# Performance work log

Measured on AMD Instinct MI355X. Metric: run time of the kernel, lower is better.

Reference implementation:

```python
import jax, jax.numpy as jnp
import numpy as np
import math

D = 768
H = 12
DK = D // H
DI = 3072
EPS_LN = 1e-12
NEG = -1e9


def layernorm(x, g, b):
    mu = jnp.mean(x, axis=-1, keepdims=True)
    var = jnp.mean(jnp.square(x - mu), axis=-1, keepdims=True)
    return (x - mu) * jax.lax.rsqrt(var + EPS_LN) * g + b


def setup_inputs() -> dict:
    key = jax.random.key(0)
    ks = jax.random.split(key, 16)
    B, S = 16, 512
    sd = 0.02
    inp = {
        "hidden_states": jax.random.normal(ks[0], (B, S, D), dtype=jnp.float32),
        "constituent_prior": jnp.zeros((B, S, S), dtype=jnp.float32),
        "attention_mask": jnp.ones((B, S), dtype=jnp.int32),
        # MultiHeadedAttention: 4 linears (q, k, v, out)
        "Wq": jax.random.normal(ks[1], (D, D)) * sd, "bq": jnp.zeros((D,)),
        "Wk": jax.random.normal(ks[2], (D, D)) * sd, "bk": jnp.zeros((D,)),
        "Wv": jax.random.normal(ks[3], (D, D)) * sd, "bv": jnp.zeros((D,)),
        "Wo": jax.random.normal(ks[4], (D, D)) * sd, "bo": jnp.zeros((D,)),
        # GroupAttention: key/query linears + LayerNorm
        "gWk": jax.random.normal(ks[5], (D, D)) * sd, "gbk": jnp.zeros((D,)),
        "gWq": jax.random.normal(ks[6], (D, D)) * sd, "gbq": jnp.zeros((D,)),
        "g_ln_g": jnp.ones((D,)), "g_ln_b": jnp.zeros((D,)),
        # BertIntermediate / BertOutput
        "Wi": jax.random.normal(ks[7], (D, DI)) * sd, "bi": jnp.zeros((DI,)),
        "Wout": jax.random.normal(ks[8], (DI, D)) * sd, "bout": jnp.zeros((D,)),
        "ln_g": jnp.ones((D,)), "ln_b": jnp.zeros((D,)),
    }
    return {k: v.astype(jnp.float32) if v.dtype == jnp.float32 or jnp.issubdtype(v.dtype, jnp.floating) else v for k, v in inp.items()}


def group_attention(x, attention_mask, prior, gWk, gbk, gWq, gbq, g_ln_g, g_ln_b):
    B, S, _ = x.shape
    a = jnp.eye(S, k=1, dtype=jnp.float32)      # super-diagonal
    c = jnp.eye(S, k=-1, dtype=jnp.float32)     # sub-diagonal
    eye = jnp.eye(S, dtype=jnp.float32)
    tri = jnp.triu(jnp.ones((S, S), dtype=jnp.float32))  # upper-tri incl. diag

    h = layernorm(x, g_ln_g, g_ln_b)
    k = h @ gWk + gbk
    q = h @ gWq + gbq
    scores = jnp.einsum("bsd,btd->bst", q, k) / D
    # mask[b,i,j] = attention_mask[b,j] & (a+c)[i,j]  (only +/-1 neighbors)
    mask = attention_mask.astype(jnp.float32)[:, None, :] * (a + c)[None]
    scores = jnp.where(mask == 0, NEG, scores)
    neigh = jax.nn.softmax(scores, axis=-1)
    neigh = jnp.sqrt(neigh * jnp.swapaxes(neigh, -2, -1) + 1e-9)
    neigh = prior + (1.0 - prior) * neigh

    # prefix log-sums along the super-diagonal via triangular matmuls
    t = jnp.where(a[None] == 0, 0.0, jnp.log(neigh + 1e-9)) @ tri
    C = jnp.exp(jnp.einsum("ij,bjk->bik", tri, t))
    C = jnp.where((tri - eye)[None] == 0, 0.0, C)   # keep strictly upper tri
    C = C + jnp.swapaxes(C, -2, -1) + jnp.where(eye[None] == 0, 1e-9, neigh)
    return C, neigh


def multi_head_attention(x, group_prob, attention_mask, Wq, bq, Wk, bk, Wv, bv, Wo, bo):
    B, S, _ = x.shape
    def split(y):  # [B,S,D] -> [B,H,S,DK]
        return y.reshape(B, S, H, DK).transpose(0, 2, 1, 3)
    q = split(x @ Wq + bq)
    k = split(x @ Wk + bk)
    v = split(x @ Wv + bv)
    scores = jnp.einsum("bhsd,bhtd->bhst", q, k) / math.sqrt(DK)
    eye = jnp.eye(S, dtype=jnp.int32)
    # combined mask: allow key j if attention_mask[b,j] or j == i (diagonal)
    cm = (attention_mask[:, None, None, :] | eye[None, None]) != 0
    scores = jnp.where(cm, scores, NEG)
    p = jax.nn.softmax(scores, axis=-1) * group_prob[:, None]  # [B,H,S,S]
    out = jnp.einsum("bhst,bhtd->bhsd", p, v)
    out = out.transpose(0, 2, 1, 3).reshape(B, S, D)
    return out @ Wo + bo


def reference(hidden_states, constituent_prior, attention_mask,
              Wq, bq, Wk, bk, Wv, bv, Wo, bo,
              gWk, gbk, gWq, gbq, g_ln_g, g_ln_b,
              Wi, bi, Wout, bout, ln_g, ln_b):
    C, neigh = group_attention(hidden_states, attention_mask, constituent_prior,
                               gWk, gbk, gWq, gbq, g_ln_g, g_ln_b)
    attn_out = multi_head_attention(hidden_states, C, attention_mask,
                                    Wq, bq, Wk, bk, Wv, bv, Wo, bo)
    inter = jax.nn.gelu(attn_out @ Wi + bi, approximate=False)
    layer_out = layernorm(inter @ Wout + bout + attn_out, ln_g, ln_b)
    return (layer_out, C, neigh, attn_out)
```

## Files before the change

### kernel.cpp

```cpp
#include <hip/hip_runtime.h>
#include <math.h>

typedef unsigned short ushort_t;
typedef __attribute__((ext_vector_type(8))) short bf16x8;
typedef __attribute__((ext_vector_type(4))) float f32x4;

#define Dt 768
#define Mrows 8192

__device__ __forceinline__ ushort_t f2b(float f) {
    union { float f; unsigned int u; } v; v.f = f;
    unsigned int u = v.u;
    unsigned int r = (u + 0x7fffu + ((u >> 16) & 1u)) >> 16;
    return (ushort_t)r;
}
__device__ __forceinline__ float b2f(ushort_t u) {
    union { unsigned int u; float f; } v; v.u = ((unsigned int)u) << 16;
    return v.f;
}
__device__ __forceinline__ f32x4 mfma16(bf16x8 a, bf16x8 b, f32x4 c) {
    return __builtin_amdgcn_mfma_f32_16x16x32_bf16(a, b, c, 0, 0, 0);
}
__device__ __forceinline__ float gelu_exact(float v) {
    return 0.5f * v * (1.0f + erff(v * 0.70710678118654752f));
}
__device__ __forceinline__ void gl2lds16(const ushort_t* g, ushort_t* l) {
    __builtin_amdgcn_global_load_lds((const __attribute__((address_space(1))) void*)g,
                                     (__attribute__((address_space(3))) void*)l,
                                     16, 0, 0);
}

__global__ __launch_bounds__(256)
void tconv6_kernel(const float* i0, const float* i1, const float* i2,
                   const float* i3, const float* i4, const float* i5,
                   ushort_t* o0, ushort_t* o1, ushort_t* o2,
                   ushort_t* o3, ushort_t* o4, ushort_t* o5)
{
    const float* in; ushort_t* out;
    switch (blockIdx.z) {
        case 0: in = i0; out = o0; break;
        case 1: in = i1; out = o1; break;
        case 2: in = i2; out = o2; break;
        case 3: in = i3; out = o3; break;
        case 4: in = i4; out = o4; break;
        default: in = i5; out = o5; break;
    }
    __shared__ float T[32][33];
    int t = threadIdx.x;
    int n0 = blockIdx.x * 32, k0 = blockIdx.y * 32;
    int r = t >> 3, c4 = (t & 7) * 4;
    float4 v = *(const float4*)(in + (size_t)(k0 + r) * 768 + n0 + c4);
    T[r][c4] = v.x; T[r][c4 + 1] = v.y; T[r][c4 + 2] = v.z; T[r][c4 + 3] = v.w;
    __syncthreads();
    int nl = t >> 3, k4 = (t & 7) * 4;
    unsigned int lo = (unsigned int)f2b(T[k4][nl]) | ((unsigned int)f2b(T[k4 + 1][nl]) << 16);
    unsigned int hi = (unsigned int)f2b(T[k4 + 2][nl]) | ((unsigned int)f2b(T[k4 + 3][nl]) << 16);
    uint2 o; o.x = lo; o.y = hi;
    *(uint2*)(out + (size_t)(n0 + nl) * 768 + k0 + k4) = o;
}

__global__ __launch_bounds__(256)
void tconv_kernel(const float* __restrict__ in, ushort_t* __restrict__ out,
                  int K, int N)
{
    __shared__ float T[32][33];
    int t = threadIdx.x;
    int n0 = blockIdx.x * 32, k0 = blockIdx.y * 32;
    int r = t >> 3, c4 = (t & 7) * 4;
    float4 v = *(const float4*)(in + (size_t)(k0 + r) * N + n0 + c4);
    T[r][c4] = v.x; T[r][c4 + 1] = v.y; T[r][c4 + 2] = v.z; T[r][c4 + 3] = v.w;
    __syncthreads();
    int nl = t >> 3, k4 = (t & 7) * 4;
    unsigned int lo = (unsigned int)f2b(T[k4][nl]) | ((unsigned int)f2b(T[k4 + 1][nl]) << 16);
    unsigned int hi = (unsigned int)f2b(T[k4 + 2][nl]) | ((unsigned int)f2b(T[k4 + 3][nl]) << 16);
    uint2 o; o.x = lo; o.y = hi;
    *(uint2*)(out + (size_t)(n0 + nl) * K + k0 + k4) = o;
}

__global__ __launch_bounds__(256)
void bconcat_kernel(const float* bq, const float* bk, const float* bv,
                    const float* gbq, const float* gbk,
                    float* bqkv, float* gbqk)
{
    int g = blockIdx.x * 256 + threadIdx.x;
    if (g < 768)       bqkv[g] = bq[g];
    else if (g < 1536) bqkv[g] = bk[g - 768];
    else if (g < 2304) bqkv[g] = bv[g - 1536];
    else if (g < 3072) gbqk[g - 2304] = gbq[g - 2304];
    else if (g < 3840) gbqk[g - 2304] = gbk[g - 3072];
}

__global__ __launch_bounds__(256)
void lnx_kernel(const float* __restrict__ x, const float* __restrict__ g,
                const float* __restrict__ be, ushort_t* __restrict__ xb,
                ushort_t* __restrict__ hb)
{
    int row = blockIdx.x;
    const float* xr = x + (size_t)row * Dt;
    int t = threadIdx.x;
    float v0 = xr[t], v1 = xr[t + 256], v2 = xr[t + 512];
    ushort_t* xrow = xb + (size_t)row * Dt;
    xrow[t] = f2b(v0); xrow[t + 256] = f2b(v1); xrow[t + 512] = f2b(v2);
    float s = v0 + v1 + v2;
    #pragma unroll
    for (int off = 32; off; off >>= 1) s += __shfl_xor(s, off, 64);
    __shared__ float r1[4], r2[4];
    if ((t & 63) == 0) r1[t >> 6] = s;
    __syncthreads();
    float mu = (r1[0] + r1[1] + r1[2] + r1[3]) * (1.0f / Dt);
    float d0 = v0 - mu, d1 = v1 - mu, d2 = v2 - mu;
    float sq = d0 * d0 + d1 * d1 + d2 * d2;
    #pragma unroll
    for (int off = 32; off; off >>= 1) sq += __shfl_xor(sq, off, 64);
    if ((t & 63) == 0) r2[t >> 6] = sq;
    __syncthreads();
    float var = (r2[0] + r2[1] + r2[2] + r2[3]) * (1.0f / Dt);
    float rs = 1.0f / sqrtf(var + 1e-12f);
    ushort_t* hrow = hb + (size_t)row * Dt;
    hrow[t]       = f2b(d0 * rs * g[t]       + be[t]);
    hrow[t + 256] = f2b(d1 * rs * g[t + 256] + be[t + 256]);
    hrow[t + 512] = f2b(d2 * rs * g[t + 512] + be[t + 512]);
}

__global__ __launch_bounds__(256)
void ln_kernel(const float* __restrict__ x, const float* __restrict__ g,
               const float* __restrict__ be, float* __restrict__ out)
{
    int row = blockIdx.x;
    const float* xr = x + (size_t)row * Dt;
    int t = threadIdx.x;
    float v0 = xr[t], v1 = xr[t + 256], v2 = xr[t + 512];
    float s = v0 + v1 + v2;
    #pragma unroll
    for (int off = 32; off; off >>= 1) s += __shfl_xor(s, off, 64);
    __shared__ float r1[4], r2[4];
    if ((t & 63) == 0) r1[t >> 6] = s;
    __syncthreads();
    float mu = (r1[0] + r1[1] + r1[2] + r1[3]) * (1.0f / Dt);
    float d0 = v0 - mu, d1 = v1 - mu, d2 = v2 - mu;
    float sq = d0 * d0 + d1 * d1 + d2 * d2;
    #pragma unroll
    for (int off = 32; off; off >>= 1) sq += __shfl_xor(sq, off, 64);
    if ((t & 63) == 0) r2[t >> 6] = sq;
    __syncthreads();
    float var = (r2[0] + r2[1] + r2[2] + r2[3]) * (1.0f / Dt);
    float rs = 1.0f / sqrtf(var + 1e-12f);
    float* orow = out + (size_t)row * Dt;
    orow[t]       = d0 * rs * g[t]       + be[t];
    orow[t + 256] = d1 * rs * g[t + 256] + be[t + 256];
    orow[t + 512] = d2 * rs * g[t + 512] + be[t + 512];
}

enum { EPI_BF16 = 1, EPI_QKV = 2, EPI_DUAL = 3, EPI_GELU = 4, EPI_RES = 5, EPI_ACC = 6 };

template<int BN, int EPI>
__global__ __launch_bounds__(256)
void gemm128(const ushort_t* __restrict__ A, const ushort_t* __restrict__ Bt,
             const float* __restrict__ bias, const float* __restrict__ res,
             float* __restrict__ Cf, ushort_t* __restrict__ O0,
             ushort_t* __restrict__ O1, ushort_t* __restrict__ O2,
             int K, int ldb, int ldc)
{
    constexpr int NF = BN / 32;
    __shared__ ushort_t As[128 * 32];
    __shared__ ushort_t Bs[BN * 32];
    int t = threadIdx.x;
    int w = t >> 6, l = t & 63;
    int wr = w >> 1, wc = w & 1;
    int lr = l & 15, lg = l >> 4;
    int bn = blockIdx.x * BN;
    int bm = blockIdx.y * 128;

    const ushort_t* gA0 = A + (size_t)(bm + (t >> 2)) * K + ((t & 3) << 3);
    const ushort_t* gA1 = A + (size_t)(bm + 64 + (t >> 2)) * K + ((t & 3) << 3);
    const ushort_t* gB0 = Bt + (size_t)(bn + (t >> 2)) * ldb + ((t & 3) << 3);
    const ushort_t* gB1 = (BN == 128) ?
        Bt + (size_t)(bn + 64 + (t >> 2)) * ldb + ((t & 3) << 3) : nullptr;
    ushort_t* lA0 = As + (w << 9);
    ushort_t* lA1 = As + 2048 + (w << 9);
    ushort_t* lB0 = Bs + (w << 9);
    ushort_t* lB1 = Bs + 2048 + (w << 9);

    f32x4 acc[4][NF];
    #pragma unroll
    for (int m = 0; m < 4; ++m)
        #pragma unroll
        for (int n = 0; n < NF; ++n) acc[m][n] = (f32x4)0.0f;

    for (int k0 = 0; k0 < K; k0 += 32) {
        gl2lds16(gA0 + k0, lA0);
        gl2lds16(gA1 + k0, lA1);
        gl2lds16(gB0 + k0, lB0);
        if (BN == 128) gl2lds16(gB1 + k0, lB1);
        __syncthreads();
        bf16x8 af[4], bfv[NF];
        #pragma unroll
        for (int m = 0; m < 4; ++m)
            af[m] = *(const bf16x8*)&As[(wr * 64 + m * 16 + lr) * 32 + lg * 8];
        #pragma unroll
        for (int n = 0; n < NF; ++n)
            bfv[n] = *(const bf16x8*)&Bs[(wc * (BN / 2) + n * 16 + lr) * 32 + lg * 8];
        __builtin_amdgcn_s_setprio(1);
        #pragma unroll
        for (int m = 0; m < 4; ++m)
            #pragma unroll
            for (int n = 0; n < NF; ++n)
                acc[m][n] = mfma16(af[m], bfv[n], acc[m][n]);
        __builtin_amdgcn_s_setprio(0);
        __syncthreads();
    }

    #pragma unroll
    for (int m = 0; m < 4; ++m) {
        int row0 = bm + wr * 64 + m * 16 + lg * 4;
        #pragma unroll
        for (int n = 0; n < NF; ++n) {
            int ng = bn + wc * (BN / 2) + n * 16 + lr;
            float v0 = acc[m][n][0], v1 = acc[m][n][1];
            float v2 = acc[m][n][2], v3 = acc[m][n][3];
            if (EPI != EPI_ACC) {
                float bv = bias[ng];
                v0 += bv; v1 += bv; v2 += bv; v3 += bv;
            }
            if (EPI == EPI_BF16) {
                O0[(size_t)(row0 + 0) * ldc + ng] = f2b(v0);
                O0[(size_t)(row0 + 1) * ldc + ng] = f2b(v1);
                O0[(size_t)(row0 + 2) * ldc + ng] = f2b(v2);
                O0[(size_t)(row0 + 3) * ldc + ng] = f2b(v3);
            } else if (EPI == EPI_QKV) {
                if (bn < 768) {
                    O0[(size_t)(row0 + 0) * 768 + ng] = f2b(v0 * 0.125f);
                    O0[(size_t)(row0 + 1) * 768 + ng] = f2b(v1 * 0.125f);
                    O0[(size_t)(row0 + 2) * 768 + ng] = f2b(v2 * 0.125f);
                    O0[(size_t)(row0 + 3) * 768 + ng] = f2b(v3 * 0.125f);
                } else if (bn < 1536) {
                    int c = ng - 768;
                    O1[(size_t)(row0 + 0) * 768 + c] = f2b(v0);
                    O1[(size_t)(row0 + 1) * 768 + c] = f2b(v1);
                    O1[(size_t)(row0 + 2) * 768 + c] = f2b(v2);
                    O1[(size_t)(row0 + 3) * 768 + c] = f2b(v3);
                } else {
                    int dk = ng - 1536;
                    unsigned int lo = (unsigned int)f2b(v0) | ((unsigned int)f2b(v1) << 16);
                    unsigned int hi = (unsigned int)f2b(v2) | ((unsigned int)f2b(v3) << 16);
                    uint2 o; o.x = lo; o.y = hi;
                    *(uint2*)(O2 + (size_t)dk * Mrows + row0) = o;
                }
            } else if (EPI == EPI_DUAL) {
                Cf[(size_t)(row0 + 0) * ldc + ng] = v0;
                Cf[(size_t)(row0 + 1) * ldc + ng] = v1;
                Cf[(size_t)(row0 + 2) * ldc + ng] = v2;
                Cf[(size_t)(row0 + 3) * ldc + ng] = v3;
                O0[(size_t)(row0 + 0) * ldc + ng] = f2b(v0);
                O0[(size_t)(row0 + 1) * ldc + ng] = f2b(v1);
                O0[(size_t)(row0 + 2) * ldc + ng] = f2b(v2);
                O0[(size_t)(row0 + 3) * ldc + ng] = f2b(v3);
            } else if (EPI == EPI_GELU) {
                O0[(size_t)(row0 + 0) * ldc + ng] = f2b(gelu_exact(v0));
                O0[(size_t)(row0 + 1) * ldc + ng] = f2b(gelu_exact(v1));
                O0[(size_t)(row0 + 2) * ldc + ng] = f2b(gelu_exact(v2));
                O0[(size_t)(row0 + 3) * ldc + ng] = f2b(gelu_exact(v3));
            } else if (EPI == EPI_RES) {
                Cf[(size_t)(row0 + 0) * ldc + ng] = v0 + res[(size_t)(row0 + 0) * Dt + ng];
                Cf[(size_t)(row0 + 1) * ldc + ng] = v1 + res[(size_t)(row0 + 1) * Dt + ng];
                Cf[(size_t)(row0 + 2) * ldc + ng] = v2 + res[(size_t)(row0 + 2) * Dt + ng];
                Cf[(size_t)(row0 + 3) * ldc + ng] = v3 + res[(size_t)(row0 + 3) * Dt + ng];
            } else if (EPI == EPI_ACC) {
                Cf[(size_t)(row0 + 0) * ldc + ng] += v0;
                Cf[(size_t)(row0 + 1) * ldc + ng] += v1;
                Cf[(size_t)(row0 + 2) * ldc + ng] += v2;
                Cf[(size_t)(row0 + 3) * ldc + ng] += v3;
            }
        }
    }
}

__global__ __launch_bounds__(256)
void group_scores_kernel(const ushort_t* __restrict__ GQK, const int* __restrict__ am,
                         float* __restrict__ smU, float* __restrict__ smD,
                         int* __restrict__ emptyF)
{
    int gi = blockIdx.x;
    int b = gi >> 9, s = gi & 511;
    int t = threadIdx.x;
    const ushort_t* qr = GQK + (size_t)gi * 1536;
    bool hasU = (s < 511) && (am[(b << 9) + s + 1] != 0);
    bool hasD = (s > 0)   && (am[(b << 9) + s - 1] != 0);
    float su = 0.0f, sd = 0.0f;
    if (hasU) {
        const ushort_t* kr = GQK + (size_t)(gi + 1) * 1536 + 768;
        for (int c = t; c < Dt; c += 256) su += b2f(qr[c]) * b2f(kr[c]);
    }
    if (hasD) {
        const ushort_t* kr = GQK + (size_t)(gi - 1) * 1536 + 768;
        for (int c = t; c < Dt; c += 256) sd += b2f(qr[c]) * b2f(kr[c]);
    }
    #pragma unroll
    for (int off = 32; off; off >>= 1) { su += __shfl_xor(su, off, 64); sd += __shfl_xor(sd, off, 64); }
    __shared__ float rU[4], rD[4];
    if ((t & 63) == 0) { rU[t >> 6] = su; rD[t >> 6] = sd; }
    __syncthreads();
    if (t == 0) {
        su = (rU[0] + rU[1] + rU[2] + rU[3]) * (1.0f / Dt);
        sd = (rD[0] + rD[1] + rD[2] + rD[3]) * (1.0f / Dt);
        float u, d2; int emp = 0;
        if (hasU && hasD) {
            float m = fmaxf(su, sd);
            float eu = __expf(su - m), ed = __expf(sd - m);
            float inv = 1.0f / (eu + ed);
            u = eu * inv; d2 = ed * inv;
        } else if (hasU) { u = 1.0f; d2 = 0.0f; }
        else if (hasD)   { u = 0.0f; d2 = 1.0f; }
        else { u = d2 = 1.0f / 512.0f; emp = 1; }
        smU[gi] = u; smD[gi] = d2; emptyF[gi] = emp;
    }
}

__global__ __launch_bounds__(64)
void prefix_kernel(const float* __restrict__ prior, const float* __restrict__ smU,
                   const float* __restrict__ smD, float* __restrict__ P)
{
    int b = blockIdx.x;
    int l = threadIdx.x;
    float lv[8];
    float run = 0.0f;
    #pragma unroll
    for (int e = 0; e < 8; ++e) {
        int j = l * 8 + e;
        float lj = 0.0f;
        if (j < 511) {
            float pr = prior[((size_t)((b << 9) + j)) * 512 + j + 1];
            float nv = pr + (1.0f - pr) *
                       sqrtf(smU[(b << 9) + j] * smD[(b << 9) + j + 1] + 1e-9f);
            lj = logf(nv + 1e-9f);
        }
        lv[e] = run;
        run += lj;
    }
    float tot = run;
    float scan = tot;
    #pragma unroll
    for (int off = 1; off < 64; off <<= 1) {
        float n = __shfl_up(scan, off, 64);
        if (l >= off) scan += n;
    }
    float excl = scan - tot;
    #pragma unroll
    for (int e = 0; e < 8; ++e)
        P[b * 512 + l * 8 + e] = excl + lv[e];
}

__global__ __launch_bounds__(512)
void neigh_cfill_kernel(const float* __restrict__ prior,
                        const float* __restrict__ smU, const float* __restrict__ smD,
                        const int* __restrict__ emptyF, const float* __restrict__ P,
                        float* __restrict__ ne_out, float* __restrict__ C_out,
                        ushort_t* __restrict__ CB)
{
    int bi = blockIdx.x;
    int j  = threadIdx.x;
    int b = bi >> 9, i = bi & 511;
    int bj = (b << 9) + j;
    const float invS = 1.0f / 512.0f;
    float fij, fji;
    if (j == i + 1)      { fij = smU[bi]; fji = smD[bj]; }
    else if (j == i - 1) { fij = smD[bi]; fji = smU[bj]; }
    else { fij = emptyF[bi] ? invS : 0.0f; fji = emptyF[bj] ? invS : 0.0f; }
    float val = sqrtf(fij * fji + 1e-9f);
    float pr = prior[(size_t)bi * 512 + j];
    float nv = pr + (1.0f - pr) * val;
    ne_out[(size_t)bi * 512 + j] = nv;
    float pi = P[bi], pj = P[bj];
    float v;
    if (j > i)      v = expf(pj - pi) + 1e-9f;
    else if (j < i) v = expf(pi - pj) + 1e-9f;
    else            v = nv;
    C_out[(size_t)bi * 512 + j] = v;
    CB[(size_t)bi * 512 + j] = f2b(v);
}

#define SMAX 12.0f
__global__ __launch_bounds__(256)
void mha_mfma(const ushort_t* __restrict__ q, const ushort_t* __restrict__ k,
              const ushort_t* __restrict__ vt, const int* __restrict__ am,
              const ushort_t* __restrict__ CB, ushort_t* __restrict__ ctx)
{
    __shared__ ushort_t Qs[64][72];
    __shared__ ushort_t Ks[64][72];
    __shared__ ushort_t Vs[64][72];
    __shared__ ushort_t Ps[64][72];
    int t = threadIdx.x;
    int w = t >> 6, l = t & 63;
    int lr = l & 15, lg = l >> 4;
    int kb8 = lg << 3;
    int qt = blockIdx.x, h = blockIdx.y, b = blockIdx.z;
    int hoff = h * 64;
    int q0 = qt * 64;
    int q0g = (b << 9) + q0;
    int myrow = w * 16 + lg * 4;

    #pragma unroll
    for (int i = 0; i < 2; ++i) {
        int c = t + i * 256;
        int r = c >> 3, dc = (c & 7) << 3;
        *(uint4*)&Qs[r][dc] = *(const uint4*)(q + (size_t)(q0g + r) * Dt + hoff + dc);
    }

    f32x4 oacc[4];
    #pragma unroll
    for (int n = 0; n < 4; ++n) oacc[n] = (f32x4)0.0f;
    float l_run[4] = {0.0f, 0.0f, 0.0f, 0.0f};

    for (int kb = 0; kb < 8; ++kb) {
        __syncthreads();
        #pragma unroll
        for (int i = 0; i < 2; ++i) {
            int c = t + i * 256;
            int r = c >> 3, dc = (c & 7) << 3;
            *(uint4*)&Ks[r][dc] =
                *(const uint4*)(k + (size_t)((b << 9) + kb * 64 + r) * Dt + hoff + dc);
            *(uint4*)&Vs[r][dc] =
                *(const uint4*)(vt + (size_t)(hoff + r) * Mrows + (b << 9) + kb * 64 + dc);
        }
        __syncthreads();

        int amv[4];
        #pragma unroll
        for (int n = 0; n < 4; ++n) amv[n] = am[(b << 9) + kb * 64 + n * 16 + lr];
        float cc[4][4];
        #pragma unroll
        for (int n = 0; n < 4; ++n)
            #pragma unroll
            for (int r = 0; r < 4; ++r)
                cc[n][r] = b2f(CB[(size_t)(q0g + myrow + r) * 512 + kb * 64 + n * 16 + lr]);

        f32x4 s[4];
        #pragma unroll
        for (int n = 0; n < 4; ++n) s[n] = (f32x4)0.0f;
        __builtin_amdgcn_s_setprio(1);
        #pragma unroll
        for (int ks = 0; ks < 2; ++ks) {
            bf16x8 aq = *(const bf16x8*)&Qs[w * 16 + lr][ks * 32 + kb8];
            #pragma unroll
            for (int n = 0; n < 4; ++n) {
                bf16x8 bk = *(const bf16x8*)&Ks[n * 16 + lr][ks * 32 + kb8];
                s[n] = mfma16(aq, bk, s[n]);
            }
        }
        __builtin_amdgcn_s_setprio(0);

        float pf[4][4];
        #pragma unroll
        for (int n = 0; n < 4; ++n) {
            int key = kb * 64 + n * 16 + lr;
            #pragma unroll
            for (int r = 0; r < 4; ++r) {
                int qrow = q0 + myrow + r;
                bool ok = (amv[n] != 0) || (key == qrow);
                float p = ok ? __expf(s[n][r] - SMAX) : 0.0f;
                pf[n][r] = p;
                l_run[r] += p;
            }
        }
        #pragma unroll
        for (int n = 0; n < 4; ++n)
            #pragma unroll
            for (int r = 0; r < 4; ++r)
                Ps[myrow + r][n * 16 + lr] = f2b(pf[n][r] * cc[n][r]);

        __builtin_amdgcn_s_setprio(1);
        #pragma unroll
        for (int ks = 0; ks < 2; ++ks) {
            bf16x8 ap = *(const bf16x8*)&Ps[w * 16 + lr][ks * 32 + kb8];
            #pragma unroll
            for (int n = 0; n < 4; ++n) {
                bf16x8 bv = *(const bf16x8*)&Vs[n * 16 + lr][ks * 32 + kb8];
                oacc[n] = mfma16(ap, bv, oacc[n]);
            }
        }
        __builtin_amdgcn_s_setprio(0);
    }
    #pragma unroll
    for (int r = 0; r < 4; ++r) {
        #pragma unroll
        for (int off = 1; off < 16; off <<= 1)
            l_run[r] += __shfl_xor(l_run[r], off, 64);
    }
    #pragma unroll
    for (int r = 0; r < 4; ++r) {
        float inv = 1.0f / l_run[r];
        #pragma unroll
        for (int n = 0; n < 4; ++n)
            ctx[(size_t)(q0g + myrow + r) * Dt + hoff + n * 16 + lr] =
                f2b(oacc[n][r] * inv);
    }
}

extern "C" void kernel_launch(void* const* d_in, const int* in_sizes, int n_in,
                              void* d_out, int out_size, void* d_ws, size_t ws_size,
                              hipStream_t stream)
{
    (void)in_sizes; (void)n_in; (void)out_size; (void)ws_size;
    const float* x     = (const float*)d_in[0];
    const float* prior = (const float*)d_in[1];
    const int*   am    = (const int*)  d_in[2];
    const float* Wq = (const float*)d_in[3];   const float* bq = (const float*)d_in[4];
    const float* Wk = (const float*)d_in[5];   const float* bk = (const float*)d_in[6];
    const float* Wv = (const float*)d_in[7];   const float* bv = (const float*)d_in[8];
    const float* Wo = (const float*)d_in[9];   const float* bo = (const float*)d_in[10];
    const float* gWk = (const float*)d_in[11]; const float* gbk = (const float*)d_in[12];
    const float* gWq = (const float*)d_in[13]; const float* gbq = (const float*)d_in[14];
    const float* glng = (const float*)d_in[15]; const float* glnb = (const float*)d_in[16];
    const float* Wi = (const float*)d_in[17];  const float* bi = (const float*)d_in[18];
    const float* Wout = (const float*)d_in[19]; const float* bout = (const float*)d_in[20];
    const float* lng = (const float*)d_in[21]; const float* lnb = (const float*)d_in[22];

    float* out = (float*)d_out;
    float* o_layer = out;
    float* o_C     = out + (size_t)6291456;
    float* o_neigh = out + (size_t)10485760;
    float* o_attn  = out + (size_t)14680064;
    ushort_t* CB = (ushort_t*)o_attn;

    char* base = (char*)d_ws;
    ushort_t* WqkvT = (ushort_t*)(base);
    ushort_t* gWqkT = (ushort_t*)(base + 3538944);
    ushort_t* WoT   = (ushort_t*)(base + 5898240);
    ushort_t* WiT   = (ushort_t*)(base + 7077888);
    ushort_t* WoutT = (ushort_t*)(base + 11796480);
    float*    bqkv  = (float*)(base + 16515072);
    float*    gbqk  = (float*)(base + 16524288);
    float*    smU   = (float*)(base + 16530432);
    float*    smD   = (float*)(base + 16563200);
    float*    Ppre  = (float*)(base + 16595968);
    int*      emptyF= (int*)(base + 16628736);
    ushort_t* s0 = (ushort_t*)(base + 16661504);
    ushort_t* s1 = (ushort_t*)(base + 29244416);
    ushort_t* s2 = (ushort_t*)(base + 41827328);
    ushort_t* XB = s0;    ushort_t* CTXB = s0;
    ushort_t* HB = s1;    ushort_t* QB = s1;   ushort_t* AB16 = s1;
    ushort_t* GQK = s2;   ushort_t* KB = s2;   ushort_t* INTER = s2;
    ushort_t* VT = s2 + 6291456;

    tconv6_kernel<<<dim3(24, 24, 6), 256, 0, stream>>>(
        Wq, Wk, Wv, gWq, gWk, Wo,
        WqkvT, WqkvT + 589824, WqkvT + 1179648, gWqkT, gWqkT + 589824, WoT);
    tconv_kernel<<<dim3(96, 24), 256, 0, stream>>>(Wi, WiT, 768, 3072);
    tconv_kernel<<<dim3(24, 96), 256, 0, stream>>>(Wout, WoutT, 3072, 768);
    bconcat_kernel<<<15, 256, 0, stream>>>(bq, bk, bv, gbq, gbk, bqkv, gbqk);

    lnx_kernel<<<8192, 256, 0, stream>>>(x, glng, glnb, XB, HB);
    gemm128<128, EPI_BF16><<<dim3(12, 64), 256, 0, stream>>>(
        HB, gWqkT, gbqk, nullptr, nullptr, GQK, nullptr, nullptr, 768, 768, 1536);
    group_scores_kernel<<<8192, 256, 0, stream>>>(GQK, am, smU, smD, emptyF);
    prefix_kernel<<<16, 64, 0, stream>>>(prior, smU, smD, Ppre);
    neigh_cfill_kernel<<<8192, 512, 0, stream>>>(prior, smU, smD, emptyF, Ppre,
                                                 o_neigh, o_C, CB);

    gemm128<128, EPI_QKV><<<dim3(18, 64), 256, 0, stream>>>(
        XB, WqkvT, bqkv, nullptr, nullptr, QB, KB, VT, 768, 768, 768);
    mha_mfma<<<dim3(8, 12, 16), 256, 0, stream>>>(QB, KB, VT, am, CB, CTXB);
    gemm128<64, EPI_DUAL><<<dim3(12, 64), 256, 0, stream>>>(
        CTXB, WoT, bo, nullptr, o_attn, AB16, nullptr, nullptr, 768, 768, 768);

    for (int c = 0; c < 2; ++c) {
        gemm128<128, EPI_GELU><<<dim3(12, 64), 256, 0, stream>>>(
            AB16, WiT + (size_t)c * 1536 * 768, bi + (size_t)c * 1536, nullptr,
            nullptr, INTER, nullptr, nullptr, 768, 768, 1536);
        if (c == 0)
            gemm128<64, EPI_RES><<<dim3(12, 64), 256, 0, stream>>>(
                INTER, WoutT + (size_t)c * 1536, bout, o_attn, o_layer, nullptr,
                nullptr, nullptr, 1536, 3072, 768);
        else
            gemm128<64, EPI_ACC><<<dim3(12, 64), 256, 0, stream>>>(
                INTER, WoutT + (size_t)c * 1536, nullptr, nullptr, o_layer, nullptr,
                nullptr, nullptr, 1536, 3072, 768);
    }
    ln_kernel<<<8192, 256, 0, stream>>>(o_layer, lng, lnb, o_layer);
}
```

Baseline: 553.9 us.

## Double-buffer GEMM LDS tiles and swizzle workgroup order across XCDs

The GEMM kernel now keeps two LDS buffers and issues the global-to-LDS loads for the next K-slice before computing on the current one. This drops one barrier per iteration and overlaps memory latency with MFMA work. Both the GEMM and the attention kernel remap block IDs so that consecutive workgroups on the same XCD handle adjacent tiles, improving L2 locality. The cost is doubled LDS use, which may reduce occupancy. The swizzle assumes the workgroup count is divisible by 8, and the single barrier relies on async load ordering being correct.

```diff
diff --git a/kernel.cpp b/kernel.cpp
--- a/kernel.cpp
+++ b/kernel.cpp
@@ -162,24 +162,28 @@
              int K, int ldb, int ldc)
 {
     constexpr int NF = BN / 32;
-    __shared__ ushort_t As[128 * 32];
-    __shared__ ushort_t Bs[BN * 32];
+    constexpr int AHALF = 128 * 32;
+    constexpr int BHALF = BN * 32;
+    __shared__ ushort_t As[2 * AHALF];
+    __shared__ ushort_t Bs[2 * BHALF];
     int t = threadIdx.x;
     int w = t >> 6, l = t & 63;
     int wr = w >> 1, wc = w & 1;
     int lr = l & 15, lg = l >> 4;
-    int bn = blockIdx.x * BN;
-    int bm = blockIdx.y * 128;
+
+    int nwg = gridDim.x * gridDim.y;
+    int bid = blockIdx.y * gridDim.x + blockIdx.x;
+    int per = nwg >> 3;
+    int sw  = (bid & 7) * per + (bid >> 3);
+    int bn = (sw % gridDim.x) * BN;
+    int bm = (sw / gridDim.x) * 128;
 
     const ushort_t* gA0 = A + (size_t)(bm + (t >> 2)) * K + ((t & 3) << 3);
     const ushort_t* gA1 = A + (size_t)(bm + 64 + (t >> 2)) * K + ((t & 3) << 3);
     const ushort_t* gB0 = Bt + (size_t)(bn + (t >> 2)) * ldb + ((t & 3) << 3);
     const ushort_t* gB1 = (BN == 128) ?
         Bt + (size_t)(bn + 64 + (t >> 2)) * ldb + ((t & 3) << 3) : nullptr;
-    ushort_t* lA0 = As + (w << 9);
-    ushort_t* lA1 = As + 2048 + (w << 9);
-    ushort_t* lB0 = Bs + (w << 9);
-    ushort_t* lB1 = Bs + 2048 + (w << 9);
+    int woff = (w << 9);
 
     f32x4 acc[4][NF];
     #pragma unroll
@@ -187,19 +191,30 @@
         #pragma unroll
         for (int n = 0; n < NF; ++n) acc[m][n] = (f32x4)0.0f;
 
+    gl2lds16(gA0, As + woff);
+    gl2lds16(gA1, As + 2048 + woff);
+    gl2lds16(gB0, Bs + woff);
+    if (BN == 128) gl2lds16(gB1, Bs + 2048 + woff);
+    __syncthreads();
+
+    int cur = 0;
     for (int k0 = 0; k0 < K; k0 += 32) {
-        gl2lds16(gA0 + k0, lA0);
-        gl2lds16(gA1 + k0, lA1);
-        gl2lds16(gB0 + k0, lB0);
-        if (BN == 128) gl2lds16(gB1 + k0, lB1);
-        __syncthreads();
+        if (k0 + 32 < K) {
+            int nb = (cur ^ 1);
+            gl2lds16(gA0 + k0 + 32, As + nb * AHALF + woff);
+            gl2lds16(gA1 + k0 + 32, As + nb * AHALF + 2048 + woff);
+            gl2lds16(gB0 + k0 + 32, Bs + nb * BHALF + woff);
+            if (BN == 128) gl2lds16(gB1 + k0 + 32, Bs + nb * BHALF + 2048 + woff);
+        }
+        const ushort_t* Ab = As + cur * AHALF;
+        const ushort_t* Bb = Bs + cur * BHALF;
         bf16x8 af[4], bfv[NF];
         #pragma unroll
         for (int m = 0; m < 4; ++m)
-            af[m] = *(const bf16x8*)&As[(wr * 64 + m * 16 + lr) * 32 + lg * 8];
+            af[m] = *(const bf16x8*)&Ab[(wr * 64 + m * 16 + lr) * 32 + lg * 8];
         #pragma unroll
         for (int n = 0; n < NF; ++n)
-            bfv[n] = *(const bf16x8*)&Bs[(wc * (BN / 2) + n * 16 + lr) * 32 + lg * 8];
+            bfv[n] = *(const bf16x8*)&Bb[(wc * (BN / 2) + n * 16 + lr) * 32 + lg * 8];
         __builtin_amdgcn_s_setprio(1);
         #pragma unroll
         for (int m = 0; m < 4; ++m)
@@ -208,6 +223,7 @@
                 acc[m][n] = mfma16(af[m], bfv[n], acc[m][n]);
         __builtin_amdgcn_s_setprio(0);
         __syncthreads();
+        cur ^= 1;
     }
 
     #pragma unroll
@@ -393,7 +409,9 @@
     int w = t >> 6, l = t & 63;
     int lr = l & 15, lg = l >> 4;
     int kb8 = lg << 3;
-    int qt = blockIdx.x, h = blockIdx.y, b = blockIdx.z;
+    int bid = (blockIdx.z * 12 + blockIdx.y) * 8 + blockIdx.x;
+    int sw = (bid & 7) * 192 + (bid >> 3);
+    int qt = sw & 7, h = (sw >> 3) % 12, b = sw / 96;
     int hoff = h * 64;
     int q0 = qt * 64;
     int q0g = (b << 9) + q0;
```

Result: faster. 523.4 us (-5.5%).
